# Kernel tuning notes

Hardware: AMD Instinct MI355X
Metric: run time of the kernel (lower is better)

The kernel has to match this reference:

```python
import jax, jax.numpy as jnp
import numpy as np
import math

B, L, D_IN, H, N, NL, D_OUT = 16, 4096, 64, 256, 32, 4, 10
EPS = 1e-5


def setup_inputs() -> dict:
    key = jax.random.key(0)
    ks = jax.random.split(key, 16)
    inp = {}
    inp['x'] = jax.random.normal(ks[0], (B, L, D_IN), dtype=jnp.float32)
    inp['enc_w'] = jax.random.normal(ks[1], (H, D_IN), dtype=jnp.float32) / math.sqrt(D_IN)
    inp['enc_b'] = jax.random.normal(ks[2], (H,), dtype=jnp.float32) * 0.01
    # log_dt uniform in [log(1e-3), log(1e-1)] as in S4D init
    inp['log_dt'] = jax.random.uniform(ks[3], (NL, H), dtype=jnp.float32,
                                       minval=math.log(1e-3), maxval=math.log(1e-1))
    inp['log_A_real'] = jnp.full((NL, H, N), math.log(0.5), dtype=jnp.float32)
    inp['A_imag'] = jnp.broadcast_to(math.pi * jnp.arange(N, dtype=jnp.float32), (NL, H, N)).copy()
    inp['C_re'] = jax.random.normal(ks[4], (NL, H, N), dtype=jnp.float32)
    inp['C_im'] = jax.random.normal(ks[5], (NL, H, N), dtype=jnp.float32)
    inp['D'] = jax.random.normal(ks[6], (NL, H), dtype=jnp.float32)
    inp['out_w'] = jax.random.normal(ks[7], (NL, 2 * H, H), dtype=jnp.float32) / math.sqrt(H)
    inp['out_b'] = jax.random.normal(ks[8], (NL, 2 * H), dtype=jnp.float32) * 0.01
    inp['ln_w'] = jnp.ones((NL, H), dtype=jnp.float32)
    inp['ln_b'] = jnp.zeros((NL, H), dtype=jnp.float32)
    inp['dec_w'] = jax.random.normal(ks[9], (D_OUT, H), dtype=jnp.float32) / math.sqrt(H)
    inp['dec_b'] = jax.random.normal(ks[10], (D_OUT,), dtype=jnp.float32) * 0.01
    return inp


def _s4d_kernel(log_dt, log_A_real, A_imag, C_re, C_im, length):
    # log_dt: (H,), others: (H, N). Returns real conv kernel (H, length).
    dt = jnp.exp(log_dt)[:, None]                       # (H, 1)
    A = -jnp.exp(log_A_real) + 1j * A_imag              # (H, N), Re(A) < 0
    dtA = A * dt                                        # (H, N)
    C = (C_re + 1j * C_im) * (jnp.expm1(dtA)) / A       # ZOH-style scaling
    t = jnp.arange(length, dtype=jnp.float32)
    vand = jnp.exp(dtA[:, :, None] * t)                 # (H, N, L) Vandermonde
    K = 2.0 * jnp.real(jnp.einsum('hn,hnl->hl', C, vand))
    return K


def _fft_conv(u, k):
    # u: (B, H, L), k: (H, L) -> causal circular-padded conv, (B, H, L)
    length = u.shape[-1]
    k_f = jnp.fft.rfft(k, n=2 * length)                 # (H, L+1)
    u_f = jnp.fft.rfft(u, n=2 * length)                 # (B, H, L+1)
    return jnp.fft.irfft(u_f * k_f[None], n=2 * length)[..., :length]


def _layernorm_channels(x, w, b):
    # x: (B, H, L), normalize over channel dim H
    mu = jnp.mean(x, axis=1, keepdims=True)
    var = jnp.var(x, axis=1, keepdims=True)
    return (x - mu) * jax.lax.rsqrt(var + EPS) * w[None, :, None] + b[None, :, None]


def reference(x, enc_w, enc_b, log_dt, log_A_real, A_imag, C_re, C_im, D,
              out_w, out_b, ln_w, ln_b, dec_w, dec_b):
    # encoder: (B, L, d_input) -> (B, L, H), then transpose -> (B, H, L)
    h = jnp.einsum('bli,hi->blh', x, enc_w) + enc_b
    h = jnp.swapaxes(h, -1, -2)                         # (B, H, L)
    length = h.shape[-1]
    for i in range(NL):
        z = h
        K = _s4d_kernel(log_dt[i], log_A_real[i], A_imag[i], C_re[i], C_im[i], length)
        y = _fft_conv(z, K) + z * D[i][None, :, None]   # SSM conv + skip
        y = jax.nn.gelu(y)
        # position-wise 1x1 conv to 2H, then GLU over channel dim
        g = jnp.einsum('bhl,gh->bgl', y, out_w[i]) + out_b[i][None, :, None]
        g1, g2 = jnp.split(g, 2, axis=1)
        y = g1 * jax.nn.sigmoid(g2)
        h = y + h                                       # residual (dropout=0)
        h = _layernorm_channels(h, ln_w[i], ln_b[i])    # post-norm
    h = jnp.swapaxes(h, -1, -2)                         # (B, L, H)
    return jnp.einsum('blh,oh->blo', h, dec_w) + dec_b
```

## Files before the change

kernel.cpp:

```cpp
#include <hip/hip_runtime.h>
#include <hip/hip_fp16.h>

#define B_   16
#define L_   4096
#define DIN  64
#define H_   256
#define N_   32
#define NL_  4
#define DOUT 10
#define CH_  32
#define T_   128

#define GAS const __attribute__((address_space(1)))
#define LAS __attribute__((address_space(3)))

typedef _Float16 half8 __attribute__((ext_vector_type(8)));
typedef _Float16 half4 __attribute__((ext_vector_type(4)));
typedef float f32x4 __attribute__((ext_vector_type(4)));

__device__ __forceinline__ float gelu_f(float v) {
    float t3  = v * v * v;
    float arg = 0.7978845608028654f * fmaf(0.044715f, t3, v);
    float e   = __expf(2.f * arg);
    float th  = 1.f - 2.f / (e + 1.f);
    return 0.5f * v * (1.f + th);
}

__global__ __launch_bounds__(256) void gen_k(
    const float* __restrict__ log_dt, const float* __restrict__ log_A_real,
    const float* __restrict__ A_imag, const float* __restrict__ C_re, const float* __restrict__ C_im,
    const float* __restrict__ Dp,
    _Float16* __restrict__ Wv, _Float16* __restrict__ Vt, _Float16* __restrict__ G,
    float* __restrict__ wtr, float* __restrict__ wti)
{
    __shared__ float sxr[N_], sxi[N_], scr[N_], sci[N_], skd[T_];
    int ih = blockIdx.x;
    int t  = threadIdx.x;
    if (t < N_) {
        int n = t;
        float dt  = expf(log_dt[ih]);
        float Are = -expf(log_A_real[ih * N_ + n]);
        float Aim = A_imag[ih * N_ + n];
        float xr = dt * Are, xi = dt * Aim;
        float ex = expf(xr), cy = cosf(xi), sy = sinf(xi);
        float sh = sinf(0.5f * xi);
        float em_re = expm1f(xr) * cy - 2.f * sh * sh;
        float em_im = ex * sy;
        float inv = 1.f / (Are * Are + Aim * Aim);
        float qr = (em_re * Are + em_im * Aim) * inv;
        float qi = (em_im * Are - em_re * Aim) * inv;
        float crv = C_re[ih * N_ + n], civ = C_im[ih * N_ + n];
        sxr[n] = xr; sxi[n] = xi;
        scr[n] = 2.f * (crv * qr - civ * qi);
        sci[n] = 2.f * (crv * qi + civ * qr);
        float txr = 128.f * xr, txi = 128.f * xi;
        float exT = expf(txr);
        wtr[ih * N_ + n] = exT * cosf(txi);
        wti[ih * N_ + n] = exT * sinf(txi);
    }
    __syncthreads();
    if (t <= T_) {
        int d = t;
        float fd = (float)d;
        float kd = 0.f;
        for (int n = 0; n < N_; n++) {
            float ar = expf(fd * sxr[n]);
            float ang = fd * sxi[n];
            float wdr = ar * cosf(ang), wdi = ar * sinf(ang);
            if (d < T_) {
                kd = fmaf(scr[n], wdr, kd);
                kd = fmaf(-sci[n], wdi, kd);
                Wv[((size_t)ih * 64 + 2 * n) * T_ + (127 - d)]     = (_Float16)wdr;
                Wv[((size_t)ih * 64 + 2 * n + 1) * T_ + (127 - d)] = (_Float16)wdi;
            }
            if (d >= 1) {
                float vr = scr[n] * wdr - sci[n] * wdi;
                float vi = scr[n] * wdi + sci[n] * wdr;
                Vt[((size_t)ih * T_ + (d - 1)) * 64 + 2 * n]     = (_Float16)vr;
                Vt[((size_t)ih * T_ + (d - 1)) * 64 + 2 * n + 1] = (_Float16)(-vi);
            }
        }
        if (d < T_) skd[d] = kd;
    }
    __syncthreads();
    if (t < T_) {
        float v = skd[127 - t];
        if (t == 127) v += Dp[ih];
        G[(size_t)ih * 256 + t]       = (_Float16)v;
        G[(size_t)ih * 256 + 128 + t] = (_Float16)0.f;
    }
}

__global__ __launch_bounds__(256) void wconv_k(const float* __restrict__ w, _Float16* __restrict__ w16)
{
    int idx = blockIdx.x * 256 + threadIdx.x;
    w16[idx] = (_Float16)w[idx];
}

__global__ __launch_bounds__(256) void dprep_k(const float* __restrict__ dw, _Float16* __restrict__ dwp)
{
    int t = threadIdx.x;
#pragma unroll
    for (int j = 0; j < 16; j++) {
        int idx = j * 256 + t;
        dwp[idx] = (idx < DOUT * H_) ? (_Float16)dw[idx] : (_Float16)0.f;
    }
}

__global__ __launch_bounds__(256) void encoder_k(
    const float* __restrict__ x, const float* __restrict__ ew,
    const float* __restrict__ eb, _Float16* __restrict__ z16)
{
    __shared__ _Float16 smem[35840];
    _Float16* xs  = smem;
    _Float16* ews = smem + 128 * 72;
    _Float16* ot  = smem;
    int b  = blockIdx.y;
    int l0 = blockIdx.x << 7;
    int t  = threadIdx.x;
#pragma unroll
    for (int j = 0; j < 8; j++) {
        int idx = j * 256 + t;
        int l = idx >> 4, i4 = (idx & 15) * 4;
        float4 v = *(const float4*)(x + ((size_t)(b * L_ + l0 + l)) * DIN + i4);
        _Float16 c[4] = {(_Float16)v.x, (_Float16)v.y, (_Float16)v.z, (_Float16)v.w};
        *(uint2*)&xs[l * 72 + i4] = *(uint2*)c;
    }
#pragma unroll
    for (int j = 0; j < 16; j++) {
        int idx = j * 256 + t;
        int h = idx >> 4, i4 = (idx & 15) * 4;
        float4 v = *(const float4*)(ew + h * 64 + i4);
        _Float16 c[4] = {(_Float16)v.x, (_Float16)v.y, (_Float16)v.z, (_Float16)v.w};
        *(uint2*)&ews[h * 72 + i4] = *(uint2*)c;
    }
    __syncthreads();
    int lane = t & 63, wid = t >> 6;
    int l15 = lane & 15, quad = lane >> 4;
    f32x4 acc[4][8];
#pragma unroll
    for (int mt = 0; mt < 4; mt++)
#pragma unroll
        for (int nt = 0; nt < 8; nt++) acc[mt][nt] = (f32x4){0.f,0.f,0.f,0.f};
#pragma unroll
    for (int ks = 0; ks < 2; ks++) {
        int kk = ks * 32 + quad * 8;
        half8 a[4], bb[8];
#pragma unroll
        for (int mt = 0; mt < 4; mt++)
            a[mt] = *(const half8*)&ews[(wid * 64 + mt * 16 + l15) * 72 + kk];
#pragma unroll
        for (int nt = 0; nt < 8; nt++)
            bb[nt] = *(const half8*)&xs[(nt * 16 + l15) * 72 + kk];
#pragma unroll
        for (int mt = 0; mt < 4; mt++)
#pragma unroll
            for (int nt = 0; nt < 8; nt++)
                acc[mt][nt] = __builtin_amdgcn_mfma_f32_16x16x32_f16(a[mt], bb[nt], acc[mt][nt], 0, 0, 0);
    }
    __syncthreads();
#pragma unroll
    for (int mt = 0; mt < 4; mt++) {
        int hb = wid * 64 + mt * 16 + quad * 4;
        float b0 = eb[hb], b1 = eb[hb + 1], b2 = eb[hb + 2], b3 = eb[hb + 3];
#pragma unroll
        for (int nt = 0; nt < 8; nt++) {
            int l = nt * 16 + l15;
            ot[(hb + 0) * 136 + l] = (_Float16)(acc[mt][nt][0] + b0);
            ot[(hb + 1) * 136 + l] = (_Float16)(acc[mt][nt][1] + b1);
            ot[(hb + 2) * 136 + l] = (_Float16)(acc[mt][nt][2] + b2);
            ot[(hb + 3) * 136 + l] = (_Float16)(acc[mt][nt][3] + b3);
        }
    }
    __syncthreads();
#pragma unroll
    for (int p = 0; p < 16; p++) {
        int row = p * 16 + (t >> 4), seg = t & 15;
        uint4 v = *(uint4*)&ot[row * 136 + seg * 8];
        *(uint4*)(z16 + ((size_t)(b * H_ + row)) * L_ + l0 + seg * 8) = v;
    }
}

__global__ __launch_bounds__(256) void finals_k(
    const _Float16* __restrict__ z16, const _Float16* __restrict__ Wv,
    const float* __restrict__ wtr, const float* __restrict__ wti,
    _Float16* __restrict__ Sinit)
{
    __shared__ _Float16 zb[CH_][136];
    __shared__ float Fs[CH_][68];
    int h = blockIdx.x, b = blockIdx.y;
    int t = threadIdx.x;
    const uint4* src = (const uint4*)(z16 + ((size_t)(b * H_ + h)) * L_);
#pragma unroll
    for (int j = 0; j < 2; j++) {
        uint4 v = src[t * 2 + j];
        int e0 = (t * 2 + j) * 8;
        *(uint4*)&zb[e0 >> 7][e0 & 127] = v;
    }
    __syncthreads();
    int lane = t & 63, w = t >> 6;
    int l15 = lane & 15, quad = lane >> 4;
    f32x4 acc[2];
    acc[0] = (f32x4){0.f,0.f,0.f,0.f};
    acc[1] = (f32x4){0.f,0.f,0.f,0.f};
    const _Float16* wvb = Wv + ((size_t)h * 64 + w * 16 + l15) * T_;
#pragma unroll
    for (int ks = 0; ks < 4; ks++) {
        int kk = ks * 32 + quad * 8;
        half8 a  = *(const half8*)(wvb + kk);
        half8 b0 = *(const half8*)&zb[l15][kk];
        half8 b1 = *(const half8*)&zb[16 + l15][kk];
        acc[0] = __builtin_amdgcn_mfma_f32_16x16x32_f16(a, b0, acc[0], 0, 0, 0);
        acc[1] = __builtin_amdgcn_mfma_f32_16x16x32_f16(a, b1, acc[1], 0, 0, 0);
    }
#pragma unroll
    for (int nt = 0; nt < 2; nt++) {
        int c = nt * 16 + l15;
        *(f32x4*)&Fs[c][w * 16 + quad * 4] = acc[nt];
    }
    __syncthreads();
    if (t < N_) {
        int n = t;
        float wr = wtr[h * N_ + n], wi = wti[h * N_ + n];
        float cr = 0.f, ci = 0.f;
        _Float16* sb = Sinit + ((size_t)(b * H_ + h)) * (CH_ * 64) + 2 * n;
        for (int c = 0; c < CH_; c++) {
            float2 f2 = *(const float2*)&Fs[c][2 * n];
            union { unsigned u; _Float16 hf[2]; } p;
            p.hf[0] = (_Float16)cr; p.hf[1] = (_Float16)ci;
            *(unsigned*)(sb + (size_t)c * 64) = p.u;
            float nr = fmaf(wr, cr, f2.x);
            nr = fmaf(-wi, ci, nr);
            float ni = fmaf(wi, cr, f2.y);
            ni = fmaf(wr, ci, ni);
            cr = nr; ci = ni;
        }
    }
}

__global__ __launch_bounds__(256, 3) void conv_k(
    const _Float16* __restrict__ z16, const _Float16* __restrict__ G,
    const _Float16* __restrict__ Vt, const _Float16* __restrict__ Sinit,
    _Float16* __restrict__ y16)
{
    __shared__ _Float16 zT[128][136];
    __shared__ _Float16 Ff[128][72];
    __shared__ _Float16 Gs[256];
    int h = blockIdx.x, rb = blockIdx.y;
    int t = threadIdx.x;
    int b0 = rb * 4;
#pragma unroll
    for (int q = 0; q < 8; q++) {
        int idx = q * 256 + t;
        int brow = idx >> 9;
        int e = (idx & 511) * 8;
        uint4 v = *(const uint4*)(z16 + ((size_t)((b0 + brow) * H_ + h)) * L_ + e);
        int c = e >> 7, jj = e & 127;
        *(uint4*)&zT[brow * 32 + c][jj] = v;
    }
#pragma unroll
    for (int q = 0; q < 4; q++) {
        int idx = q * 256 + t;
        int e0 = idx * 8;
        int brow = e0 >> 11;
        int off = e0 & 2047;
        uint4 v = *(const uint4*)(Sinit + ((size_t)((b0 + brow) * H_ + h)) * (CH_ * 64) + off);
        int r = brow * 32 + (off >> 6), k = off & 63;
        *(uint4*)&Ff[r][k] = v;
    }
    Gs[t] = G[(size_t)h * 256 + t];
    __syncthreads();
    int lane = t & 63, w = t >> 6;
    int l15 = lane & 15, quad = lane >> 4;
    f32x4 acc[2][8];
#pragma unroll
    for (int mt = 0; mt < 2; mt++)
#pragma unroll
        for (int nt = 0; nt < 8; nt++) acc[mt][nt] = (f32x4){0.f,0.f,0.f,0.f};
#pragma unroll
    for (int ks = 0; ks < 4; ks++) {
        int kk = ks * 32 + quad * 8;
        int base0 = 127 - (w * 32 + l15) + kk;
        int base1 = base0 - 16;
        half8 a0, a1;
#pragma unroll
        for (int j = 0; j < 8; j++) { a0[j] = Gs[base0 + j]; a1[j] = Gs[base1 + j]; }
#pragma unroll
        for (int nt = 0; nt < 8; nt++) {
            half8 bf = *(const half8*)&zT[nt * 16 + l15][kk];
            acc[0][nt] = __builtin_amdgcn_mfma_f32_16x16x32_f16(a0, bf, acc[0][nt], 0, 0, 0);
            acc[1][nt] = __builtin_amdgcn_mfma_f32_16x16x32_f16(a1, bf, acc[1][nt], 0, 0, 0);
        }
    }
    const _Float16* vb = Vt + (size_t)h * T_ * 64;
#pragma unroll
    for (int ks = 0; ks < 2; ks++) {
        int kk = ks * 32 + quad * 8;
        half8 a0 = *(const half8*)(vb + ((size_t)(w * 32 + l15)) * 64 + kk);
        half8 a1 = *(const half8*)(vb + ((size_t)(w * 32 + 16 + l15)) * 64 + kk);
#pragma unroll
        for (int nt = 0; nt < 8; nt++) {
            half8 bf = *(const half8*)&Ff[nt * 16 + l15][kk];
            acc[0][nt] = __builtin_amdgcn_mfma_f32_16x16x32_f16(a0, bf, acc[0][nt], 0, 0, 0);
            acc[1][nt] = __builtin_amdgcn_mfma_f32_16x16x32_f16(a1, bf, acc[1][nt], 0, 0, 0);
        }
    }
    __syncthreads();
#pragma unroll
    for (int mt = 0; mt < 2; mt++)
#pragma unroll
        for (int nt = 0; nt < 8; nt++) {
            int r = nt * 16 + l15;
            int tt0 = w * 32 + mt * 16 + quad * 4;
            _Float16 o[4];
#pragma unroll
            for (int rr = 0; rr < 4; rr++) o[rr] = (_Float16)gelu_f(acc[mt][nt][rr]);
            *(uint2*)&zT[r][tt0] = *(uint2*)o;
        }
    __syncthreads();
#pragma unroll
    for (int q = 0; q < 8; q++) {
        int idx = q * 256 + t;
        int brow = idx >> 9;
        int e = (idx & 511) * 8;
        int c = e >> 7, jj = e & 127;
        uint4 v = *(uint4*)&zT[brow * 32 + c][jj];
        *(uint4*)(y16 + ((size_t)((b0 + brow) * H_ + h)) * L_ + e) = v;
    }
}

__global__ __launch_bounds__(256, 2) void glu_k(
    const _Float16* __restrict__ W, const _Float16* __restrict__ y16,
    const float* __restrict__ outb, const float* __restrict__ lnw,
    const float* __restrict__ lnb, _Float16* __restrict__ z16)
{
    __shared__ __align__(16) _Float16 yT_u[64 * 266];
    __shared__ __align__(16) _Float16 zs[256 * 64];
    __shared__ float red[2][4][64];
    __shared__ float mus[64], rss[64];
    _Float16* yT = yT_u;
    _Float16* us = yT_u;
    int b  = blockIdx.y;
    int l0 = blockIdx.x << 6;
    int t  = threadIdx.x;
    int lane = t & 63, wid = t >> 6;
    int l15 = lane & 15, quad = lane >> 4;
    {
        const uint4* src = (const uint4*)(y16 + ((size_t)(b * H_ + t)) * L_ + l0);
        uint4 v[8];
#pragma unroll
        for (int j = 0; j < 8; j++) v[j] = src[j];
        {
            int rsub = lane >> 3, csub = (lane & 7) * 8;
#pragma unroll
            for (int q = 0; q < 8; q++) {
                int ch = wid * 64 + q * 8 + rsub;
                const _Float16* gp = z16 + ((size_t)(b * H_ + ch)) * L_ + l0 + csub;
                __builtin_amdgcn_global_load_lds((GAS unsigned*)(const void*)gp,
                                                 (LAS unsigned*)(void*)&zs[(wid * 64 + q * 8) * 64],
                                                 16, 0, 0);
            }
        }
        const _Float16* hv = (const _Float16*)v;
#pragma unroll
        for (int j = 0; j < 64; j++) yT[j * 266 + t] = hv[j];
    }
    __syncthreads();
    f32x4 acc[8][4];
#pragma unroll
    for (int mt = 0; mt < 8; mt++)
#pragma unroll
        for (int nt = 0; nt < 4; nt++) acc[mt][nt] = (f32x4){0.f,0.f,0.f,0.f};
#pragma unroll
    for (int ks = 0; ks < 8; ks++) {
        int kk = ks * 32 + quad * 8;
        half8 bf[4];
#pragma unroll
        for (int nt = 0; nt < 4; nt++) bf[nt] = *(const half8*)&yT[(nt * 16 + l15) * 266 + kk];
#pragma unroll
        for (int mt = 0; mt < 8; mt++) {
            int row = (mt >> 2) * 256 + wid * 64 + (mt & 3) * 16 + l15;
            half8 a = *(const half8*)(W + (size_t)row * H_ + kk);
#pragma unroll
            for (int nt = 0; nt < 4; nt++)
                acc[mt][nt] = __builtin_amdgcn_mfma_f32_16x16x32_f16(a, bf[nt], acc[mt][nt], 0, 0, 0);
        }
    }
    __syncthreads();
#pragma unroll
    for (int mt = 0; mt < 4; mt++) {
        int chb = wid * 64 + mt * 16 + quad * 4;
        float4 ob1 = *(const float4*)(outb + chb);
        float4 ob2 = *(const float4*)(outb + 256 + chb);
        const float* o1 = (const float*)&ob1;
        const float* o2 = (const float*)&ob2;
#pragma unroll
        for (int nt = 0; nt < 4; nt++) {
            int l = nt * 16 + l15;
#pragma unroll
            for (int r = 0; r < 4; r++) {
                float g1 = acc[mt][nt][r] + o1[r];
                float g2 = acc[mt + 4][nt][r] + o2[r];
                float sg = 1.f / (1.f + __expf(-g2));
                us[(chb + r) * 66 + l] = (_Float16)(g1 * sg);
            }
        }
    }
    __syncthreads();
    int lr = t & 63, grp = t >> 6;
    float s1 = 0.f, s2 = 0.f;
    for (int j = 0; j < 64; j++) {
        int ch = grp * 64 + j;
        float uu = (float)us[ch * 66 + lr] + (float)zs[ch * 64 + lr];
        us[ch * 66 + lr] = (_Float16)uu;
        s1 += uu; s2 = fmaf(uu, uu, s2);
    }
    red[0][grp][lr] = s1; red[1][grp][lr] = s2;
    __syncthreads();
    if (t < 64) {
        float a = red[0][0][t] + red[0][1][t] + red[0][2][t] + red[0][3][t];
        float q = red[1][0][t] + red[1][1][t] + red[1][2][t] + red[1][3][t];
        float mu  = a * (1.f / 256.f);
        float var = q * (1.f / 256.f) - mu * mu;
        mus[t] = mu; rss[t] = rsqrtf(var + 1e-5f);
    }
    __syncthreads();
    int lg = (t & 15) * 4, ch0 = t >> 4;
    float mu4[4], rs4[4];
#pragma unroll
    for (int i = 0; i < 4; i++) { mu4[i] = mus[lg + i]; rs4[i] = rss[lg + i]; }
#pragma unroll
    for (int j = 0; j < 16; j++) {
        int ch = ch0 + 16 * j;
        float wv = lnw[ch], bv = lnb[ch];
        _Float16 o4[4];
#pragma unroll
        for (int i = 0; i < 4; i++) {
            float vv = ((float)us[ch * 66 + lg + i] - mu4[i]) * rs4[i] * wv + bv;
            o4[i] = (_Float16)vv;
        }
        *(uint2*)(z16 + ((size_t)(b * H_ + ch)) * L_ + l0 + lg) = *(uint2*)o4;
    }
}

__global__ __launch_bounds__(256) void decoder_k(
    const _Float16* __restrict__ z16, const _Float16* __restrict__ dwp,
    const float* __restrict__ db, float* __restrict__ out)
{
    __shared__ _Float16 zT[128][268];
    int b  = blockIdx.y;
    int l0 = blockIdx.x << 7;
    int t  = threadIdx.x;
#pragma unroll 8
    for (int j = 0; j < 64; j++) {
        int idx = j * 256 + t;
        int h = idx >> 6, lp = idx & 63;
        unsigned v = *(const unsigned*)(z16 + ((size_t)(b * H_ + h)) * L_ + l0 + lp * 2);
        union { unsigned u; _Float16 f[2]; } c; c.u = v;
        zT[lp * 2][h]     = c.f[0];
        zT[lp * 2 + 1][h] = c.f[1];
    }
    __syncthreads();
    int lane = t & 63, wid = t >> 6;
    int l15 = lane & 15, quad = lane >> 4;
    f32x4 acc[2];
    acc[0] = (f32x4){0.f,0.f,0.f,0.f};
    acc[1] = (f32x4){0.f,0.f,0.f,0.f};
#pragma unroll
    for (int ks = 0; ks < 8; ks++) {
        int kk = ks * 32 + quad * 8;
        half8 a = *(const half8*)(dwp + l15 * 256 + kk);
#pragma unroll
        for (int nt = 0; nt < 2; nt++) {
            int l = (wid * 2 + nt) * 16 + l15;
            half4 lo = *(const half4*)&zT[l][kk];
            half4 hi = *(const half4*)&zT[l][kk + 4];
            half8 bf;
#pragma unroll
            for (int j = 0; j < 4; j++) { bf[j] = lo[j]; bf[j + 4] = hi[j]; }
            acc[nt] = __builtin_amdgcn_mfma_f32_16x16x32_f16(a, bf, acc[nt], 0, 0, 0);
        }
    }
    int o0 = quad * 4;
#pragma unroll
    for (int nt = 0; nt < 2; nt++) {
        int l = (wid * 2 + nt) * 16 + l15;
        float* op = out + ((size_t)(b * L_ + l0 + l)) * DOUT;
#pragma unroll
        for (int r = 0; r < 4; r++) {
            int o = o0 + r;
            if (o < DOUT) op[o] = acc[nt][r] + db[o];
        }
    }
}

extern "C" void kernel_launch(void* const* d_in, const int* in_sizes, int n_in,
                              void* d_out, int out_size, void* d_ws, size_t ws_size,
                              hipStream_t stream)
{
    (void)in_sizes; (void)n_in; (void)out_size; (void)ws_size;
    const float* x          = (const float*)d_in[0];
    const float* enc_w      = (const float*)d_in[1];
    const float* enc_b      = (const float*)d_in[2];
    const float* log_dt     = (const float*)d_in[3];
    const float* log_A_real = (const float*)d_in[4];
    const float* A_imag     = (const float*)d_in[5];
    const float* C_re       = (const float*)d_in[6];
    const float* C_im       = (const float*)d_in[7];
    const float* Dp         = (const float*)d_in[8];
    const float* out_w      = (const float*)d_in[9];
    const float* out_b      = (const float*)d_in[10];
    const float* ln_w       = (const float*)d_in[11];
    const float* ln_b       = (const float*)d_in[12];
    const float* dec_w      = (const float*)d_in[13];
    const float* dec_b      = (const float*)d_in[14];
    float* outp = (float*)d_out;

    char* ws = (char*)d_ws;
    _Float16* z16 = (_Float16*)ws;   ws += (size_t)B_ * H_ * L_ * 2;
    _Float16* y16 = (_Float16*)ws;   ws += (size_t)B_ * H_ * L_ * 2;
    _Float16* Sinit = (_Float16*)ws; ws += (size_t)B_ * H_ * CH_ * 64 * 2;
    _Float16* Wv = (_Float16*)ws;    ws += (size_t)NL_ * H_ * 64 * T_ * 2;
    _Float16* Vt = (_Float16*)ws;    ws += (size_t)NL_ * H_ * T_ * 64 * 2;
    _Float16* G  = (_Float16*)ws;    ws += (size_t)NL_ * H_ * 256 * 2;
    size_t tb = (size_t)NL_ * H_ * N_;
    float* wtr = (float*)ws; ws += tb * 4;
    float* wti = (float*)ws; ws += tb * 4;
    _Float16* W16 = (_Float16*)ws; ws += (size_t)NL_ * 2 * H_ * H_ * 2;
    _Float16* dwp = (_Float16*)ws; ws += (size_t)16 * H_ * 2;

    gen_k<<<NL_ * H_, 256, 0, stream>>>(log_dt, log_A_real, A_imag, C_re, C_im, Dp,
                                        Wv, Vt, G, wtr, wti);
    wconv_k<<<(NL_ * 2 * H_ * H_) / 256, 256, 0, stream>>>(out_w, W16);
    dprep_k<<<1, 256, 0, stream>>>(dec_w, dwp);
    encoder_k<<<dim3(L_ / 128, B_), 256, 0, stream>>>(x, enc_w, enc_b, z16);
    for (int i = 0; i < NL_; i++) {
        size_t th = (size_t)i * H_;
        finals_k<<<dim3(H_, B_), 256, 0, stream>>>(z16, Wv + th * 64 * T_,
                                                   wtr + th * N_, wti + th * N_, Sinit);
        conv_k<<<dim3(H_, B_ / 4), 256, 0, stream>>>(z16, G + th * 256, Vt + th * T_ * 64,
                                                     Sinit, y16);
        glu_k<<<dim3(L_ / 64, B_), 256, 0, stream>>>(W16 + (size_t)i * 2 * H_ * H_, y16,
                                                     out_b + i * 2 * H_, ln_w + th, ln_b + th, z16);
    }
    decoder_k<<<dim3(L_ / 128, B_), 256, 0, stream>>>(z16, dwp, dec_b, outp);
}
```

Before: 537.7 us.

## Fuse chunk-final state computation into the SSM convolution kernel

Removes the separate finals_k launch and its Sinit global buffer. conv2_k now computes the per-chunk final states with MFMA from the z tile it already holds in LDS, runs the 32-step complex state recurrence per wave, and writes the results straight into the Ff shared buffer. This avoids re-reading z16 from global memory, the Sinit write and read round-trip, and one launch per layer. In exchange, each conv block does a serial recurrence that only 32 lanes per wave perform, and it adds extra syncs that lengthen the block. The recurrence inputs are now stored as fp16 in LDS rather than fp32, which lowers precision slightly.

```diff
diff --git a/kernel.cpp b/kernel.cpp
--- a/kernel.cpp
+++ b/kernel.cpp
@@ -181,66 +181,10 @@
     }
 }
 
-__global__ __launch_bounds__(256) void finals_k(
-    const _Float16* __restrict__ z16, const _Float16* __restrict__ Wv,
+__global__ __launch_bounds__(256, 3) void conv2_k(
+    const _Float16* __restrict__ z16, const _Float16* __restrict__ G,
+    const _Float16* __restrict__ Vt, const _Float16* __restrict__ Wv,
     const float* __restrict__ wtr, const float* __restrict__ wti,
-    _Float16* __restrict__ Sinit)
-{
-    __shared__ _Float16 zb[CH_][136];
-    __shared__ float Fs[CH_][68];
-    int h = blockIdx.x, b = blockIdx.y;
-    int t = threadIdx.x;
-    const uint4* src = (const uint4*)(z16 + ((size_t)(b * H_ + h)) * L_);
-#pragma unroll
-    for (int j = 0; j < 2; j++) {
-        uint4 v = src[t * 2 + j];
-        int e0 = (t * 2 + j) * 8;
-        *(uint4*)&zb[e0 >> 7][e0 & 127] = v;
-    }
-    __syncthreads();
-    int lane = t & 63, w = t >> 6;
-    int l15 = lane & 15, quad = lane >> 4;
-    f32x4 acc[2];
-    acc[0] = (f32x4){0.f,0.f,0.f,0.f};
-    acc[1] = (f32x4){0.f,0.f,0.f,0.f};
-    const _Float16* wvb = Wv + ((size_t)h * 64 + w * 16 + l15) * T_;
-#pragma unroll
-    for (int ks = 0; ks < 4; ks++) {
-        int kk = ks * 32 + quad * 8;
-        half8 a  = *(const half8*)(wvb + kk);
-        half8 b0 = *(const half8*)&zb[l15][kk];
-        half8 b1 = *(const half8*)&zb[16 + l15][kk];
-        acc[0] = __builtin_amdgcn_mfma_f32_16x16x32_f16(a, b0, acc[0], 0, 0, 0);
-        acc[1] = __builtin_amdgcn_mfma_f32_16x16x32_f16(a, b1, acc[1], 0, 0, 0);
-    }
-#pragma unroll
-    for (int nt = 0; nt < 2; nt++) {
-        int c = nt * 16 + l15;
-        *(f32x4*)&Fs[c][w * 16 + quad * 4] = acc[nt];
-    }
-    __syncthreads();
-    if (t < N_) {
-        int n = t;
-        float wr = wtr[h * N_ + n], wi = wti[h * N_ + n];
-        float cr = 0.f, ci = 0.f;
-        _Float16* sb = Sinit + ((size_t)(b * H_ + h)) * (CH_ * 64) + 2 * n;
-        for (int c = 0; c < CH_; c++) {
-            float2 f2 = *(const float2*)&Fs[c][2 * n];
-            union { unsigned u; _Float16 hf[2]; } p;
-            p.hf[0] = (_Float16)cr; p.hf[1] = (_Float16)ci;
-            *(unsigned*)(sb + (size_t)c * 64) = p.u;
-            float nr = fmaf(wr, cr, f2.x);
-            nr = fmaf(-wi, ci, nr);
-            float ni = fmaf(wi, cr, f2.y);
-            ni = fmaf(wr, ci, ni);
-            cr = nr; ci = ni;
-        }
-    }
-}
-
-__global__ __launch_bounds__(256, 3) void conv_k(
-    const _Float16* __restrict__ z16, const _Float16* __restrict__ G,
-    const _Float16* __restrict__ Vt, const _Float16* __restrict__ Sinit,
     _Float16* __restrict__ y16)
 {
     __shared__ _Float16 zT[128][136];
@@ -258,20 +202,59 @@
         int c = e >> 7, jj = e & 127;
         *(uint4*)&zT[brow * 32 + c][jj] = v;
     }
-#pragma unroll
-    for (int q = 0; q < 4; q++) {
-        int idx = q * 256 + t;
-        int e0 = idx * 8;
-        int brow = e0 >> 11;
-        int off = e0 & 2047;
-        uint4 v = *(const uint4*)(Sinit + ((size_t)((b0 + brow) * H_ + h)) * (CH_ * 64) + off);
-        int r = brow * 32 + (off >> 6), k = off & 63;
-        *(uint4*)&Ff[r][k] = v;
-    }
     Gs[t] = G[(size_t)h * 256 + t];
     __syncthreads();
     int lane = t & 63, w = t >> 6;
     int l15 = lane & 15, quad = lane >> 4;
+    {
+        f32x4 facc[4][2];
+#pragma unroll
+        for (int mt = 0; mt < 4; mt++) {
+            facc[mt][0] = (f32x4){0.f,0.f,0.f,0.f};
+            facc[mt][1] = (f32x4){0.f,0.f,0.f,0.f};
+        }
+        const _Float16* wvb = Wv + (size_t)h * 64 * T_;
+#pragma unroll
+        for (int ks = 0; ks < 4; ks++) {
+            int kk = ks * 32 + quad * 8;
+            half8 bf0 = *(const half8*)&zT[w * 32 + l15][kk];
+            half8 bf1 = *(const half8*)&zT[w * 32 + 16 + l15][kk];
+#pragma unroll
+            for (int mt = 0; mt < 4; mt++) {
+                half8 a = *(const half8*)(wvb + (size_t)(mt * 16 + l15) * T_ + kk);
+                facc[mt][0] = __builtin_amdgcn_mfma_f32_16x16x32_f16(a, bf0, facc[mt][0], 0, 0, 0);
+                facc[mt][1] = __builtin_amdgcn_mfma_f32_16x16x32_f16(a, bf1, facc[mt][1], 0, 0, 0);
+            }
+        }
+#pragma unroll
+        for (int mt = 0; mt < 4; mt++)
+#pragma unroll
+            for (int nt = 0; nt < 2; nt++) {
+                int cr = w * 32 + nt * 16 + l15;
+                int cc = mt * 16 + quad * 4;
+#pragma unroll
+                for (int r = 0; r < 4; r++)
+                    Ff[cr][cc + r] = (_Float16)facc[mt][nt][r];
+            }
+    }
+    __syncthreads();
+    if (lane < 32) {
+        int n = lane;
+        float wr = wtr[h * N_ + n], wi = wti[h * N_ + n];
+        float cr = 0.f, ci = 0.f;
+        for (int c = 0; c < CH_; c++) {
+            float fr = (float)Ff[w * 32 + c][2 * n];
+            float fi = (float)Ff[w * 32 + c][2 * n + 1];
+            Ff[w * 32 + c][2 * n]     = (_Float16)cr;
+            Ff[w * 32 + c][2 * n + 1] = (_Float16)ci;
+            float nr = fmaf(wr, cr, fr);
+            nr = fmaf(-wi, ci, nr);
+            float ni = fmaf(wi, cr, fi);
+            ni = fmaf(wr, ci, ni);
+            cr = nr; ci = ni;
+        }
+    }
+    __syncthreads();
     f32x4 acc[2][8];
 #pragma unroll
     for (int mt = 0; mt < 2; mt++)
@@ -519,7 +502,6 @@
     char* ws = (char*)d_ws;
     _Float16* z16 = (_Float16*)ws;   ws += (size_t)B_ * H_ * L_ * 2;
     _Float16* y16 = (_Float16*)ws;   ws += (size_t)B_ * H_ * L_ * 2;
-    _Float16* Sinit = (_Float16*)ws; ws += (size_t)B_ * H_ * CH_ * 64 * 2;
     _Float16* Wv = (_Float16*)ws;    ws += (size_t)NL_ * H_ * 64 * T_ * 2;
     _Float16* Vt = (_Float16*)ws;    ws += (size_t)NL_ * H_ * T_ * 64 * 2;
     _Float16* G  = (_Float16*)ws;    ws += (size_t)NL_ * H_ * 256 * 2;
@@ -536,10 +518,9 @@
     encoder_k<<<dim3(L_ / 128, B_), 256, 0, stream>>>(x, enc_w, enc_b, z16);
     for (int i = 0; i < NL_; i++) {
         size_t th = (size_t)i * H_;
-        finals_k<<<dim3(H_, B_), 256, 0, stream>>>(z16, Wv + th * 64 * T_,
-                                                   wtr + th * N_, wti + th * N_, Sinit);
-        conv_k<<<dim3(H_, B_ / 4), 256, 0, stream>>>(z16, G + th * 256, Vt + th * T_ * 64,
-                                                     Sinit, y16);
+        conv2_k<<<dim3(H_, B_ / 4), 256, 0, stream>>>(z16, G + th * 256, Vt + th * T_ * 64,
+                                                      Wv + th * 64 * T_, wtr + th * N_, wti + th * N_,
+                                                      y16);
         glu_k<<<dim3(L_ / 64, B_), 256, 0, stream>>>(W16 + (size_t)i * 2 * H_ * H_, y16,
                                                      out_b + i * 2 * H_, ln_w + th, ln_b + th, z16);
     }
```

Result: faster. 516.0 us (-4.0%).
